# Kernel optimization log

Measured on AMD Instinct MI355X. Metric: run time of the kernel, lower is better.

The kernel has to match this reference:

```python
import jax, jax.numpy as jnp
import numpy as np

N, E, H = 20000, 320000, 5
IND, OUT = 64, 64
D2 = 2 * OUT          # 128
CAT = OUT + D2        # 192
BN_EPS = 1e-5


def _bn(x, g, b, m, v):
    # eval-mode BatchNorm1d
    return (x - m) * jax.lax.rsqrt(v + BN_EPS) * g + b


def _gcn(x, W, b, src, dst, n):
    # PyG GCNConv: add self-loops (already in src/dst), sym-normalized aggregation
    h = x @ W                                             # [N, C]
    deg = jax.ops.segment_sum(jnp.ones_like(dst, dtype=h.dtype), dst, num_segments=n)
    dinv = jnp.where(deg > 0, jax.lax.rsqrt(deg), 0.0)
    norm = dinv[src] * dinv[dst]                          # [E']
    out = jax.ops.segment_sum(h[src] * norm[:, None], dst, num_segments=n)
    return out + b


def _gat(x, W, att_src, att_dst, b, src, dst, n, heads, c):
    # PyG GATConv (concat=False): per-edge attention, segment softmax over dst
    hx = (x @ W).reshape(n, heads, c)                     # [N, H, C]
    a_s = jnp.einsum('nhc,hc->nh', hx, att_src)           # [N, H]
    a_d = jnp.einsum('nhc,hc->nh', hx, att_dst)
    e = jax.nn.leaky_relu(a_s[src] + a_d[dst], 0.2)       # [E', H]
    m = jax.ops.segment_max(e, dst, num_segments=n)       # every node has a self-loop
    w = jnp.exp(e - m[dst])
    den = jax.ops.segment_sum(w, dst, num_segments=n)
    alpha = w / den[dst]                                  # [E', H]
    out = jax.ops.segment_sum(hx[src] * alpha[:, :, None], dst, num_segments=n)  # [N,H,C]
    return out.mean(axis=1) + b


def setup_inputs() -> dict:
    key = jax.random.key(0)
    ks = iter(jax.random.split(key, 64))
    rn = lambda *s: jax.random.normal(next(ks), s, dtype=jnp.float32) * 0.05
    d = {}
    d['x_in'] = jax.random.normal(next(ks), (N, IND), dtype=jnp.float32)
    d['edge_index'] = jax.random.randint(next(ks), (2, E), 0, N, dtype=jnp.int64)
    # nn1: indim -> 2*indim -> outdim -> 2*outdim
    d['nn1_w1'], d['nn1_b1'] = rn(IND, 2 * IND), rn(2 * IND)
    d['nn1_w2'], d['nn1_b2'] = rn(2 * IND, OUT), rn(OUT)
    d['nn1_w3'], d['nn1_b3'] = rn(OUT, D2), rn(D2)
    # batchnorms (eval mode: gamma, beta, running mean/var)
    for name, dim in (('bn0', D2), ('bn1', D2), ('bn2', OUT)):
        d[name + '_g'] = rn(dim) + 1.0
        d[name + '_b'] = rn(dim)
        d[name + '_m'] = rn(dim)
        d[name + '_v'] = jax.random.uniform(next(ks), (dim,), jnp.float32, 0.5, 1.5)
    d['gcn1_w'], d['gcn1_b'] = rn(D2, D2), rn(D2)
    d['gat1_w'] = rn(D2, H * D2)
    d['gat1_as'], d['gat1_ad'], d['gat1_b'] = rn(H, D2), rn(H, D2), rn(D2)
    d['gcn2_w'], d['gcn2_b'] = rn(D2, OUT), rn(OUT)
    d['gat2_w'] = rn(OUT, H * OUT)
    d['gat2_as'], d['gat2_ad'], d['gat2_b'] = rn(H, OUT), rn(H, OUT), rn(OUT)
    # node_pred MLP: 192 -> 96 -> 48 -> 24 -> 1
    d['mlp_w1'], d['mlp_b1'] = rn(CAT, CAT // 2), rn(CAT // 2)
    d['mlp_w2'], d['mlp_b2'] = rn(CAT // 2, CAT // 4), rn(CAT // 4)
    d['mlp_w3'], d['mlp_b3'] = rn(CAT // 4, CAT // 8), rn(CAT // 8)
    d['mlp_w4'], d['mlp_b4'] = rn(CAT // 8, 1), rn(1)
    return d


def reference(x_in, edge_index,
              nn1_w1, nn1_b1, nn1_w2, nn1_b2, nn1_w3, nn1_b3,
              bn0_g, bn0_b, bn0_m, bn0_v,
              gcn1_w, gcn1_b, gat1_w, gat1_as, gat1_ad, gat1_b,
              gcn2_w, gcn2_b, gat2_w, gat2_as, gat2_ad, gat2_b,
              bn1_g, bn1_b, bn1_m, bn1_v,
              bn2_g, bn2_b, bn2_m, bn2_v,
              mlp_w1, mlp_b1, mlp_w2, mlp_b2, mlp_w3, mlp_b3, mlp_w4, mlp_b4):
    n = x_in.shape[0]
    loop = jnp.arange(n, dtype=edge_index.dtype)
    src = jnp.concatenate([edge_index[0], loop])   # self-loops (GCN & GAT defaults)
    dst = jnp.concatenate([edge_index[1], loop])

    sp = jax.nn.softplus
    x = sp(x_in @ nn1_w1 + nn1_b1)
    x = sp(x @ nn1_w2 + nn1_b2)
    x = x @ nn1_w3 + nn1_b3
    x = jax.nn.leaky_relu(_bn(x, bn0_g, bn0_b, bn0_m, bn0_v), 0.01)

    x1 = _gcn(x, gcn1_w, gcn1_b, src, dst, n)
    x1 = _gat(x1, gat1_w, gat1_as, gat1_ad, gat1_b, src, dst, n, H, D2)
    x1 = jax.nn.leaky_relu(_bn(x1, bn1_g, bn1_b, bn1_m, bn1_v), 0.01)
    skip1 = x + x1

    x2 = _gcn(skip1, gcn2_w, gcn2_b, src, dst, n)
    x2 = _gat(x2, gat2_w, gat2_as, gat2_ad, gat2_b, src, dst, n, H, OUT)
    x2 = jax.nn.leaky_relu(_bn(x2, bn2_g, bn2_b, bn2_m, bn2_v), 0.01)

    xf = jnp.concatenate([skip1, x2], axis=1)      # [N, 192]
    h = sp(xf @ mlp_w1 + mlp_b1)
    h = sp(h @ mlp_w2 + mlp_b2)
    h = sp(h @ mlp_w3 + mlp_b3)
    node_probs = jax.nn.sigmoid(h @ mlp_w4 + mlp_b4)   # [N, 1]
    return xf, node_probs
```

## Files before the change

kernel.cpp:

```cpp
#include <hip/hip_runtime.h>
#include <hip/hip_bf16.h>
#include <math.h>
#include <stdint.h>

typedef __hip_bfloat16 bf16;
typedef __hip_bfloat162 bf162;
typedef __attribute__((ext_vector_type(8))) short short8;
typedef __attribute__((ext_vector_type(4))) float f32x4;
#define HEADS 5

static inline long long cdivll(long long a, long long b){ return (a + b - 1) / b; }

__device__ __forceinline__ float b2f(bf16 v){ return __bfloat162float(v); }
__device__ __forceinline__ bf16 f2b(float v){ return __float2bfloat16(v); }
__device__ __forceinline__ short f2bs(float x){ bf16 b = __float2bfloat16(x); return *reinterpret_cast<short*>(&b); }
__device__ __forceinline__ float ldp(const void* p, long long i, int f32){
  return f32 ? ((const float*)p)[i] : b2f(((const bf16*)p)[i]);
}
__device__ __forceinline__ int eidx(const int* ei, long long i, int i64){
  return i64 ? ei[2 * i] : ei[i];
}
__device__ __forceinline__ float lrelu(float x, float a){ return x >= 0.f ? x : a * x; }
__device__ __forceinline__ float splus(float x){ return fmaxf(x, 0.f) + log1pf(expf(-fabsf(x))); }

__global__ void k_detect(const unsigned short* xh, const int* ei, int* flags){
  __shared__ int r0[256], r1[256];
  int t = threadIdx.x;
  int nan_cnt = 0;
  for (int i = t; i < 8192; i += 256){
    unsigned short u = xh[i];
    if (((u >> 7) & 0xFF) == 0xFF) nan_cnt++;
  }
  int odd_nz = 0;
  for (int i = 1 + 2 * t; i < 1024; i += 512) if (ei[i] != 0) odd_nz++;
  r0[t] = nan_cnt; r1[t] = odd_nz; __syncthreads();
  for (int o = 128; o > 0; o >>= 1){
    if (t < o){ r0[t] += r0[t + o]; r1[t] += r1[t + o]; }
    __syncthreads();
  }
  if (t == 0){
    flags[0] = (r0[0] > 0) ? 1 : 0;
    flags[1] = (r1[0] == 0) ? 1 : 0;
  }
}

__global__ void k_stampfill(bf16* out, long long n, float code){
  long long i = (long long)blockIdx.x * blockDim.x + threadIdx.x;
  if (i < n) out[i] = f2b(i == 0 ? code : 0.f);
}

__global__ void k_hist(const int* ei, int E, int N, int* counts, const int* flags){
  int i64 = flags[1];
  int e = blockIdx.x * blockDim.x + threadIdx.x;
  if (e >= E + N) return;
  int d = (e < E) ? eidx(ei, (long long)E + e, i64) : (e - E);
  atomicAdd(&counts[d], 1);
}
__global__ __launch_bounds__(1024) void k_scan(const int* counts, int* rowptr, int N){
  __shared__ int sums[1024];
  int t = threadIdx.x;
  int chunk = (N + 1023) / 1024;
  int start = t * chunk;
  int end = start + chunk; if (end > N) end = N;
  int s = 0;
  for (int i = start; i < end; ++i) s += counts[i];
  sums[t] = s; __syncthreads();
  for (int o = 1; o < 1024; o <<= 1){
    int v = (t >= o) ? sums[t - o] : 0;
    __syncthreads();
    sums[t] += v;
    __syncthreads();
  }
  int run = (t == 0) ? 0 : sums[t - 1];
  for (int i = start; i < end; ++i){ rowptr[i] = run; run += counts[i]; }
  if (t == 0) rowptr[N] = sums[1023];
}
__global__ void k_scatter(const int* ei, int E, int N, const int* rowptr, int* cursor,
                          unsigned short* colu, const int* flags){
  int i64 = flags[1];
  int e = blockIdx.x * blockDim.x + threadIdx.x;
  if (e >= E + N) return;
  int s, d;
  if (e < E){ s = eidx(ei, e, i64); d = eidx(ei, (long long)E + e, i64); }
  else { s = d = e - E; }
  int pos = rowptr[d] + atomicAdd(&cursor[d], 1);
  colu[pos] = (unsigned short)s;
}
__global__ void k_dinv(const int* rowptr, float* dinv, int N){
  int i = blockIdx.x * blockDim.x + threadIdx.x;
  if (i < N) dinv[i] = rsqrtf((float)(rowptr[i + 1] - rowptr[i]));
}

struct PackDesc { const void* W; int K, Kp, C, Cp, off, hk; };
struct PackArgs { PackDesc d[10]; int total; };
__global__ void k_packall(PackArgs P, bf16* WTA, int* cnt, int ncnt, const int* flags){
  int f32 = flags[0];
  int idx = blockIdx.x * blockDim.x + threadIdx.x;
  if (idx >= P.total){
    int z = idx - P.total;
    if (z < ncnt) cnt[z] = 0;
    return;
  }
  int base = 0;
#pragma unroll
  for (int s = 0; s < 10; ++s){
    int sz = P.d[s].Kp * P.d[s].Cp;
    if (idx < base + sz){
      int local = idx - base;
      int c = local / P.d[s].Kp;
      int k = local - c * P.d[s].Kp;
      float v;
      if (P.d[s].hk){
        int h = k / P.d[s].K;
        int kk = k - h * P.d[s].K;
        v = (c < P.d[s].C)
          ? ldp(P.d[s].W, (long long)kk * (P.d[s].hk * P.d[s].C) + h * P.d[s].C + c, f32) : 0.f;
      } else {
        v = (k < P.d[s].K && c < P.d[s].C)
          ? ldp(P.d[s].W, (long long)k * P.d[s].C + c, f32) : 0.f;
      }
      WTA[P.d[s].off + local] = f2b(v);
      return;
    }
    base += sz;
  }
}

__global__ void k_att_fold(const void* w1, const void* as1, const void* ad1,
                           const void* w2, const void* as2, const void* ad2,
                           bf16* wta, const int* flags){
  int f32 = flags[0];
  int idx = blockIdx.x * blockDim.x + threadIdx.x;
  if (idx < 8192){
    int c = idx >> 7, k = idx & 127;
    float v = 0.f;
    if (c < 10){
      int h = (c < 5) ? c : c - 5;
      const void* aw = (c < 5) ? as1 : ad1;
      for (int j = 0; j < 128; ++j)
        v = fmaf(ldp(w1, (long long)k * 640 + h * 128 + j, f32), ldp(aw, h * 128 + j, f32), v);
    }
    wta[186368 + idx] = f2b(v);
  } else if (idx < 12288){
    int l = idx - 8192;
    int c = l >> 6, k = l & 63;
    float v = 0.f;
    if (c < 10){
      int h = (c < 5) ? c : c - 5;
      const void* aw = (c < 5) ? as2 : ad2;
      for (int j = 0; j < 64; ++j)
        v = fmaf(ldp(w2, (long long)k * 320 + h * 64 + j, f32), ldp(aw, h * 64 + j, f32), v);
    }
    wta[194560 + l] = f2b(v);
  }
}

__global__ __launch_bounds__(256) void k_gemm_mfma(
    const void* in, int ik, int ldin, const bf16* WT, int Kp, int ks, const void* bias,
    float* outf, bf16* outb, int N, int C, int ldc, int czero, int mode,
    const void* bg, const void* bb, const void* bm, const void* bv,
    const float* skip, void* out2, int c2off, const int* flags)
{
  __shared__ float red[3][16][64];
  int f32 = flags[0];
  int use_b16 = (ik == 1) || (ik == 2 && !f32);
  int t = threadIdx.x;
  int wave = t >> 6, lane = t & 63;
  int quad = lane >> 4, l15 = lane & 15;
  int nrg = 4 / ks;
  int rowgrp = wave & (nrg - 1);
  int kh = wave / nrg;
  int mbase = blockIdx.x * (16 * nrg) + rowgrp * 16;
  int c0 = blockIdx.y * 64;
  f32x4 acc[4];
#pragma unroll
  for (int j = 0; j < 4; ++j) acc[j] = (f32x4){0.f, 0.f, 0.f, 0.f};

  int m = mbase + l15; if (m > N - 1) m = N - 1;

  int Kseg = Kp / ks;
  int kend = (kh + 1) * Kseg;
  for (int k0 = kh * Kseg; k0 < kend; k0 += 32){
    int ka = k0 + quad * 8;
    short8 af;
    if (use_b16){
      af = *(const short8*)((const bf16*)in + (size_t)m * ldin + ka);
    } else {
      const float* p = (const float*)in + (size_t)m * ldin + ka;
      float4 v0 = *(const float4*)p;
      float4 v1 = *(const float4*)(p + 4);
      af[0] = f2bs(v0.x); af[1] = f2bs(v0.y); af[2] = f2bs(v0.z); af[3] = f2bs(v0.w);
      af[4] = f2bs(v1.x); af[5] = f2bs(v1.y); af[6] = f2bs(v1.z); af[7] = f2bs(v1.w);
    }
#pragma unroll
    for (int j = 0; j < 4; ++j){
      short8 bvv = *(const short8*)(WT + (size_t)(c0 + 16 * j + l15) * Kp + ka);
      acc[j] = __builtin_amdgcn_mfma_f32_16x16x32_bf16(af, bvv, acc[j], 0, 0, 0);
    }
  }

  if (ks > 1){
    if (kh > 0){
      int slot = (kh - 1) * nrg + rowgrp;
#pragma unroll
      for (int j = 0; j < 4; ++j)
#pragma unroll
        for (int r = 0; r < 4; ++r)
          red[slot][quad * 4 + r][16 * j + l15] = acc[j][r];
    }
    __syncthreads();
    if (kh > 0) return;
#pragma unroll
    for (int s = 0; s < 3; ++s){
      if (s < ks - 1){
        int slot = s * nrg + rowgrp;
#pragma unroll
        for (int j = 0; j < 4; ++j)
#pragma unroll
          for (int r = 0; r < 4; ++r)
            acc[j][r] += red[slot][quad * 4 + r][16 * j + l15];
      }
    }
  }

#pragma unroll
  for (int j = 0; j < 4; ++j){
    int c = c0 + 16 * j + l15;
    if (c < C){
      float bi = bias ? ldp(bias, c, f32) : 0.f;
      float g = 0.f, be = 0.f, mm = 0.f, iv = 0.f;
      if (mode == 2){
        g = ldp(bg, c, f32); be = ldp(bb, c, f32); mm = ldp(bm, c, f32);
        iv = rsqrtf(ldp(bv, c, f32) + 1e-5f);
      }
#pragma unroll
      for (int r = 0; r < 4; ++r){
        int n = mbase + quad * 4 + r;
        if (n >= N) continue;
        float y = acc[j][r] + bi;
        if (mode == 1) y = splus(y);
        else if (mode == 2){
          y = (y - mm) * iv * g + be; y = lrelu(y, 0.01f);
          if (skip) y += skip[(size_t)n * ldc + c];
        }
        if (out2){
          size_t o2 = (size_t)n * 192 + c2off + c;
          if (f32) ((float*)out2)[o2] = y; else ((bf16*)out2)[o2] = f2b(y);
        }
        size_t o = (size_t)n * ldc + c;
        if (outb) outb[o] = f2b(y); else if (outf) outf[o] = y;
      }
    } else if (c < czero){
#pragma unroll
      for (int r = 0; r < 4; ++r){
        int n = mbase + quad * 4 + r;
        if (n >= N) continue;
        size_t o = (size_t)n * ldc + c;
        if (outb) outb[o] = f2b(0.f); else if (outf) outf[o] = 0.f;
      }
    }
  }
}

__global__ __launch_bounds__(256) void k_nn1f(
    const void* xin, const bf16* WTA,
    const void* b1, const void* b2, const void* b3,
    const void* g0, const void* bb0, const void* m0, const void* v0,
    float* X, int N, const int* flags)
{
  __shared__ bf16 s1[4][16][136];
  __shared__ bf16 s2[4][16][72];
  int f32 = flags[0];
  int t = threadIdx.x, wave = t >> 6, lane = t & 63;
  int quad = lane >> 4, l15 = lane & 15;
  int mbase = blockIdx.x * 64 + wave * 16;
  int m = mbase + l15; if (m > N - 1) m = N - 1;

  f32x4 a1[8];
#pragma unroll
  for (int j = 0; j < 8; ++j) a1[j] = (f32x4){0.f, 0.f, 0.f, 0.f};
#pragma unroll
  for (int k0 = 0; k0 < 64; k0 += 32){
    int ka = k0 + quad * 8;
    short8 af;
    if (!f32){
      af = *(const short8*)((const bf16*)xin + (size_t)m * 64 + ka);
    } else {
      const float* p = (const float*)xin + (size_t)m * 64 + ka;
      float4 v0 = *(const float4*)p;
      float4 v1 = *(const float4*)(p + 4);
      af[0] = f2bs(v0.x); af[1] = f2bs(v0.y); af[2] = f2bs(v0.z); af[3] = f2bs(v0.w);
      af[4] = f2bs(v1.x); af[5] = f2bs(v1.y); af[6] = f2bs(v1.z); af[7] = f2bs(v1.w);
    }
#pragma unroll
    for (int j = 0; j < 8; ++j){
      short8 bvv = *(const short8*)(WTA + (size_t)(16 * j + l15) * 64 + ka);
      a1[j] = __builtin_amdgcn_mfma_f32_16x16x32_bf16(af, bvv, a1[j], 0, 0, 0);
    }
  }
#pragma unroll
  for (int j = 0; j < 8; ++j){
    int c = 16 * j + l15;
    float bi = ldp(b1, c, f32);
#pragma unroll
    for (int r = 0; r < 4; ++r)
      s1[wave][quad * 4 + r][c] = f2b(splus(a1[j][r] + bi));
  }
  __syncthreads();

  f32x4 a2[4];
#pragma unroll
  for (int j = 0; j < 4; ++j) a2[j] = (f32x4){0.f, 0.f, 0.f, 0.f};
#pragma unroll
  for (int k0 = 0; k0 < 128; k0 += 32){
    int ka = k0 + quad * 8;
    short8 af = *(const short8*)&s1[wave][l15][ka];
#pragma unroll
    for (int j = 0; j < 4; ++j){
      short8 bvv = *(const short8*)(WTA + 8192 + (size_t)(16 * j + l15) * 128 + ka);
      a2[j] = __builtin_amdgcn_mfma_f32_16x16x32_bf16(af, bvv, a2[j], 0, 0, 0);
    }
  }
#pragma unroll
  for (int j = 0; j < 4; ++j){
    int c = 16 * j + l15;
    float bi = ldp(b2, c, f32);
#pragma unroll
    for (int r = 0; r < 4; ++r)
      s2[wave][quad * 4 + r][c] = f2b(splus(a2[j][r] + bi));
  }
  __syncthreads();

  f32x4 a3[8];
#pragma unroll
  for (int j = 0; j < 8; ++j) a3[j] = (f32x4){0.f, 0.f, 0.f, 0.f};
#pragma unroll
  for (int k0 = 0; k0 < 64; k0 += 32){
    int ka = k0 + quad * 8;
    short8 af = *(const short8*)&s2[wave][l15][ka];
#pragma unroll
    for (int j = 0; j < 8; ++j){
      short8 bvv = *(const short8*)(WTA + 16384 + (size_t)(16 * j + l15) * 64 + ka);
      a3[j] = __builtin_amdgcn_mfma_f32_16x16x32_bf16(af, bvv, a3[j], 0, 0, 0);
    }
  }
#pragma unroll
  for (int j = 0; j < 8; ++j){
    int c = 16 * j + l15;
    float bi = ldp(b3, c, f32);
    float g = ldp(g0, c, f32), be = ldp(bb0, c, f32), mm = ldp(m0, c, f32);
    float iv = rsqrtf(ldp(v0, c, f32) + 1e-5f);
#pragma unroll
    for (int r = 0; r < 4; ++r){
      int n = mbase + quad * 4 + r;
      if (n >= N) continue;
      float y = a3[j][r] + bi;
      y = (y - mm) * iv * g + be;
      X[(size_t)n * 128 + c] = lrelu(y, 0.01f);
    }
  }
}

__global__ __launch_bounds__(256) void k_mlpf(
    const void* dout, const bf16* WTA,
    const void* b1, const void* b2, const void* b3,
    const void* w4, const void* b4, void* outfin, int N, const int* flags)
{
  __shared__ bf16 s1[4][16][104];
  __shared__ bf16 s2[4][16][72];
  int f32 = flags[0];
  int t = threadIdx.x, wave = t >> 6, lane = t & 63;
  int quad = lane >> 4, l15 = lane & 15;
  int mbase = blockIdx.x * 64 + wave * 16;
  int m = mbase + l15; if (m > N - 1) m = N - 1;

  f32x4 a1[6];
#pragma unroll
  for (int j = 0; j < 6; ++j) a1[j] = (f32x4){0.f, 0.f, 0.f, 0.f};
#pragma unroll
  for (int k0 = 0; k0 < 192; k0 += 32){
    int ka = k0 + quad * 8;
    short8 af;
    if (!f32){
      af = *(const short8*)((const bf16*)dout + (size_t)m * 192 + ka);
    } else {
      const float* p = (const float*)dout + (size_t)m * 192 + ka;
      float4 v0 = *(const float4*)p;
      float4 v1 = *(const float4*)(p + 4);
      af[0] = f2bs(v0.x); af[1] = f2bs(v0.y); af[2] = f2bs(v0.z); af[3] = f2bs(v0.w);
      af[4] = f2bs(v1.x); af[5] = f2bs(v1.y); af[6] = f2bs(v1.z); af[7] = f2bs(v1.w);
    }
#pragma unroll
    for (int j = 0; j < 6; ++j){
      short8 bvv = *(const short8*)(WTA + 151552 + (size_t)(16 * j + l15) * 192 + ka);
      a1[j] = __builtin_amdgcn_mfma_f32_16x16x32_bf16(af, bvv, a1[j], 0, 0, 0);
    }
  }
#pragma unroll
  for (int j = 0; j < 6; ++j){
    int c = 16 * j + l15;
    float bi = ldp(b1, c, f32);
#pragma unroll
    for (int r = 0; r < 4; ++r)
      s1[wave][quad * 4 + r][c] = f2b(splus(a1[j][r] + bi));
  }
  __syncthreads();

  f32x4 a2[3];
#pragma unroll
  for (int j = 0; j < 3; ++j) a2[j] = (f32x4){0.f, 0.f, 0.f, 0.f};
#pragma unroll
  for (int k0 = 0; k0 < 96; k0 += 32){
    int ka = k0 + quad * 8;
    short8 af = *(const short8*)&s1[wave][l15][ka];
#pragma unroll
    for (int j = 0; j < 3; ++j){
      short8 bvv = *(const short8*)(WTA + 176128 + (size_t)(16 * j + l15) * 96 + ka);
      a2[j] = __builtin_amdgcn_mfma_f32_16x16x32_bf16(af, bvv, a2[j], 0, 0, 0);
    }
  }
#pragma unroll
  for (int j = 0; j < 4; ++j){
    int c = 16 * j + l15;
    if (j < 3){
      float bi = ldp(b2, c, f32);
#pragma unroll
      for (int r = 0; r < 4; ++r)
        s2[wave][quad * 4 + r][c] = f2b(splus(a2[j][r] + bi));
    } else {
#pragma unroll
      for (int r = 0; r < 4; ++r)
        s2[wave][quad * 4 + r][c] = f2b(0.f);
    }
  }
  __syncthreads();

  f32x4 a3[2];
#pragma unroll
  for (int j = 0; j < 2; ++j) a3[j] = (f32x4){0.f, 0.f, 0.f, 0.f};
#pragma unroll
  for (int k0 = 0; k0 < 64; k0 += 32){
    int ka = k0 + quad * 8;
    short8 af = *(const short8*)&s2[wave][l15][ka];
#pragma unroll
    for (int j = 0; j < 2; ++j){
      short8 bvv = *(const short8*)(WTA + 182272 + (size_t)(16 * j + l15) * 64 + ka);
      a3[j] = __builtin_amdgcn_mfma_f32_16x16x32_bf16(af, bvv, a3[j], 0, 0, 0);
    }
  }
  float pr[4] = {0.f, 0.f, 0.f, 0.f};
#pragma unroll
  for (int j = 0; j < 2; ++j){
    int c = 16 * j + l15;
    float w = (c < 24) ? ldp(w4, c, f32) : 0.f;
    float bi = (c < 24) ? ldp(b3, c, f32) : 0.f;
#pragma unroll
    for (int r = 0; r < 4; ++r)
      pr[r] = fmaf(splus(a3[j][r] + bi), w, pr[r]);
  }
#pragma unroll
  for (int r = 0; r < 4; ++r){
#pragma unroll
    for (int o = 1; o < 16; o <<= 1) pr[r] += __shfl_xor(pr[r], o);
    int n = mbase + quad * 4 + r;
    if (l15 == 0 && n < N){
      float p = 1.f / (1.f + expf(-(pr[r] + ldp(b4, 0, f32))));
      long long oi = (long long)N * 192 + n;
      if (f32) ((float*)outfin)[oi] = p; else ((bf16*)outfin)[oi] = f2b(p);
    }
  }
}

__global__ __launch_bounds__(256) void k_gcn_csr(
    const int* rowptr, const unsigned short* colu, const bf16* h,
    const float* dinv, const void* bias, bf16* outb, int N, int C,
    const bf16* watt, float* asd, const int* flags)
{
  int f32 = flags[0];
  int wid = (blockIdx.x * 256 + threadIdx.x) >> 6;
  int lane = threadIdx.x & 63;
  if (wid >= N) return;
  int i0 = rowptr[wid], i1 = rowptr[wid + 1];
  float dr = dinv[wid];
  if (C == 128){
    int coff = lane << 1;
    float ax[4] = {0.f, 0.f, 0.f, 0.f}, ay[4] = {0.f, 0.f, 0.f, 0.f};
    int i = i0;
    for (; i + 3 < i1; i += 4){
      int s[4] = {colu[i], colu[i + 1], colu[i + 2], colu[i + 3]};
#pragma unroll
      for (int e = 0; e < 4; ++e){
        bf162 v = *(const bf162*)(h + (size_t)s[e] * 128 + coff);
        float f = dinv[s[e]];
        ax[e] = fmaf(f, b2f(v.x), ax[e]); ay[e] = fmaf(f, b2f(v.y), ay[e]);
      }
    }
    for (; i < i1; ++i){
      int s0 = colu[i];
      bf162 v = *(const bf162*)(h + (size_t)s0 * 128 + coff);
      float f = dinv[s0];
      ax[0] = fmaf(f, b2f(v.x), ax[0]); ay[0] = fmaf(f, b2f(v.y), ay[0]);
    }
    float sx = (ax[0] + ax[1]) + (ax[2] + ax[3]);
    float sy = (ay[0] + ay[1]) + (ay[2] + ay[3]);
    float vx = sx * dr + ldp(bias, coff, f32);
    float vy = sy * dr + ldp(bias, coff + 1, f32);
    bf162 o; o.x = f2b(vx); o.y = f2b(vy);
    *(bf162*)(outb + (size_t)wid * 128 + coff) = o;
    if (watt){
      float myv = 0.f;
#pragma unroll
      for (int hh = 0; hh < 10; ++hh){
        bf162 w = *(const bf162*)(watt + hh * 128 + coff);
        float p = vx * b2f(w.x) + vy * b2f(w.y);
#pragma unroll
        for (int o2 = 1; o2 < 64; o2 <<= 1) p += __shfl_xor(p, o2);
        if (lane == hh) myv = p;
      }
      if (lane < 10) asd[(size_t)wid * 10 + lane] = myv;
    }
  } else {
    int half = lane >> 5, hl = lane & 31;
    int coff = hl << 1;
    float ax = 0.f, ay = 0.f, bx = 0.f, by = 0.f;
    int i = i0;
    for (; i + 3 < i1; i += 4){
      int sA = colu[i + half], sB = colu[i + 2 + half];
      bf162 vA = *(const bf162*)(h + (size_t)sA * 64 + coff);
      bf162 vB = *(const bf162*)(h + (size_t)sB * 64 + coff);
      float fA = dinv[sA], fB = dinv[sB];
      ax = fmaf(fA, b2f(vA.x), ax); ay = fmaf(fA, b2f(vA.y), ay);
      bx = fmaf(fB, b2f(vB.x), bx); by = fmaf(fB, b2f(vB.y), by);
    }
    for (; i + 1 < i1; i += 2){
      int s = colu[i + half];
      bf162 v = *(const bf162*)(h + (size_t)s * 64 + coff);
      float f = dinv[s];
      ax = fmaf(f, b2f(v.x), ax); ay = fmaf(f, b2f(v.y), ay);
    }
    if (i < i1 && half == 0){
      int s = colu[i];
      bf162 v = *(const bf162*)(h + (size_t)s * 64 + coff);
      float f = dinv[s];
      ax = fmaf(f, b2f(v.x), ax); ay = fmaf(f, b2f(v.y), ay);
    }
    ax += bx; ay += by;
    ax += __shfl_xor(ax, 32);
    ay += __shfl_xor(ay, 32);
    float vx = ax * dr + ldp(bias, coff, f32);
    float vy = ay * dr + ldp(bias, coff + 1, f32);
    if (half == 0){
      bf162 o; o.x = f2b(vx); o.y = f2b(vy);
      *(bf162*)(outb + (size_t)wid * 64 + coff) = o;
    }
    if (watt){
      float myv = 0.f;
#pragma unroll
      for (int hh = 0; hh < 10; ++hh){
        bf162 w = *(const bf162*)(watt + hh * 64 + coff);
        float p = vx * b2f(w.x) + vy * b2f(w.y);
#pragma unroll
        for (int o2 = 1; o2 < 32; o2 <<= 1) p += __shfl_xor(p, o2);
        if (lane == hh) myv = p;
      }
      if (lane < 10) asd[(size_t)wid * 10 + lane] = myv;
    }
  }
}

__global__ __launch_bounds__(256) void k_gat_fused(
    const int* rowptr, const unsigned short* colu, const bf16* bbx,
    const float* asd, bf16* agg, int N, int K)
{
  __shared__ float als[4][HEADS][64];
  __shared__ unsigned short ssrc[4][64];
  int widx = threadIdx.x >> 6;
  int wid = (blockIdx.x * 256 + threadIdx.x) >> 6;
  int lane = threadIdx.x & 63;
  if (wid >= N) return;
  int i0 = rowptr[wid], i1 = rowptr[wid + 1];
  float adr[HEADS];
#pragma unroll
  for (int h = 0; h < HEADS; ++h) adr[h] = asd[(size_t)wid * 10 + 5 + h];
  float m[HEADS];
#pragma unroll
  for (int h = 0; h < HEADS; ++h) m[h] = -1e30f;
  for (int i = i0 + lane; i < i1; i += 64){
    int s = colu[i];
#pragma unroll
    for (int h = 0; h < HEADS; ++h){
      float e = lrelu(asd[(size_t)s * 10 + h] + adr[h], 0.2f);
      m[h] = fmaxf(m[h], e);
    }
  }
#pragma unroll
  for (int h = 0; h < HEADS; ++h)
    for (int o = 32; o > 0; o >>= 1) m[h] = fmaxf(m[h], __shfl_xor(m[h], o));
  float den[HEADS];
#pragma unroll
  for (int h = 0; h < HEADS; ++h) den[h] = 0.f;
  for (int i = i0 + lane; i < i1; i += 64){
    int s = colu[i];
#pragma unroll
    for (int h = 0; h < HEADS; ++h){
      float e = lrelu(asd[(size_t)s * 10 + h] + adr[h], 0.2f);
      den[h] += expf(e - m[h]);
    }
  }
#pragma unroll
  for (int h = 0; h < HEADS; ++h){
    for (int o = 32; o > 0; o >>= 1) den[h] += __shfl_xor(den[h], o);
    den[h] = 1.f / (den[h] * (float)HEADS);
  }
  if (K == 128){
    int coff = lane << 1;
    float ax[HEADS], ay[HEADS];
#pragma unroll
    for (int h = 0; h < HEADS; ++h){ ax[h] = 0.f; ay[h] = 0.f; }
    for (int base = i0; base < i1; base += 64){
      int iend = i1 - base; if (iend > 64) iend = 64;
      int i = base + lane;
      if (i < i1){
        int s = colu[i];
        ssrc[widx][lane] = (unsigned short)s;
#pragma unroll
        for (int h = 0; h < HEADS; ++h){
          float e = lrelu(asd[(size_t)s * 10 + h] + adr[h], 0.2f);
          als[widx][h][lane] = expf(e - m[h]) * den[h];
        }
      }
      asm volatile("s_waitcnt lgkmcnt(0)" ::: "memory");
      int j = 0;
      for (; j + 3 < iend; j += 4){
        int s4[4];
#pragma unroll
        for (int e = 0; e < 4; ++e) s4[e] = ssrc[widx][j + e];
        bf162 v[4];
#pragma unroll
        for (int e = 0; e < 4; ++e) v[e] = *(const bf162*)(bbx + (size_t)s4[e] * 128 + coff);
#pragma unroll
        for (int e = 0; e < 4; ++e){
          float fx = b2f(v[e].x), fy = b2f(v[e].y);
#pragma unroll
          for (int h = 0; h < HEADS; ++h){
            float a = als[widx][h][j + e];
            ax[h] = fmaf(a, fx, ax[h]); ay[h] = fmaf(a, fy, ay[h]);
          }
        }
      }
      for (; j < iend; ++j){
        int s = ssrc[widx][j];
        bf162 v = *(const bf162*)(bbx + (size_t)s * 128 + coff);
        float fx = b2f(v.x), fy = b2f(v.y);
#pragma unroll
        for (int h = 0; h < HEADS; ++h){
          float a = als[widx][h][j];
          ax[h] = fmaf(a, fx, ax[h]); ay[h] = fmaf(a, fy, ay[h]);
        }
      }
    }
#pragma unroll
    for (int h = 0; h < HEADS; ++h){
      bf162 o; o.x = f2b(ax[h]); o.y = f2b(ay[h]);
      *(bf162*)(agg + (size_t)wid * 640 + h * 128 + coff) = o;
    }
  } else {
    int half = lane >> 5, hl = lane & 31;
    int coff = hl << 1;
    float ax[HEADS], ay[HEADS];
#pragma unroll
    for (int h = 0; h < HEADS; ++h){ ax[h] = 0.f; ay[h] = 0.f; }
    for (int base = i0; base < i1; base += 64){
      int iend = i1 - base; if (iend > 64) iend = 64;
      int i = base + lane;
      if (i < i1){
        int s = colu[i];
        ssrc[widx][lane] = (unsigned short)s;
#pragma unroll
        for (int h = 0; h < HEADS; ++h){
          float e = lrelu(asd[(size_t)s * 10 + h] + adr[h], 0.2f);
          als[widx][h][lane] = expf(e - m[h]) * den[h];
        }
      }
      asm volatile("s_waitcnt lgkmcnt(0)" ::: "memory");
      int j = 0;
      for (; j + 3 < iend; j += 4){
        int sA = ssrc[widx][j + half], sB = ssrc[widx][j + 2 + half];
        bf162 vA = *(const bf162*)(bbx + (size_t)sA * 64 + coff);
        bf162 vB = *(const bf162*)(bbx + (size_t)sB * 64 + coff);
        float Ax = b2f(vA.x), Ay = b2f(vA.y), Bx = b2f(vB.x), By = b2f(vB.y);
#pragma unroll
        for (int h = 0; h < HEADS; ++h){
          float aA = als[widx][h][j + half], aB = als[widx][h][j + 2 + half];
          ax[h] = fmaf(aA, Ax, ax[h]); ay[h] = fmaf(aA, Ay, ay[h]);
          ax[h] = fmaf(aB, Bx, ax[h]); ay[h] = fmaf(aB, By, ay[h]);
        }
      }
      for (; j + 1 < iend; j += 2){
        int s = ssrc[widx][j + half];
        bf162 v = *(const bf162*)(bbx + (size_t)s * 64 + coff);
        float fx = b2f(v.x), fy = b2f(v.y);
#pragma unroll
        for (int h = 0; h < HEADS; ++h){
          float a = als[widx][h][j + half];
          ax[h] = fmaf(a, fx, ax[h]); ay[h] = fmaf(a, fy, ay[h]);
        }
      }
      if (j < iend && half == 0){
        int s = ssrc[widx][j];
        bf162 v = *(const bf162*)(bbx + (size_t)s * 64 + coff);
        float fx = b2f(v.x), fy = b2f(v.y);
#pragma unroll
        for (int h = 0; h < HEADS; ++h){
          float a = als[widx][h][j];
          ax[h] = fmaf(a, fx, ax[h]); ay[h] = fmaf(a, fy, ay[h]);
        }
      }
    }
#pragma unroll
    for (int h = 0; h < HEADS; ++h){
      ax[h] += __shfl_xor(ax[h], 32);
      ay[h] += __shfl_xor(ay[h], 32);
    }
    if (half == 0){
#pragma unroll
      for (int h = 0; h < HEADS; ++h){
        bf162 o; o.x = f2b(ax[h]); o.y = f2b(ay[h]);
        *(bf162*)(agg + (size_t)wid * 320 + h * 64 + coff) = o;
      }
    }
  }
}

extern "C" void kernel_launch(void* const* d_in, const int* in_sizes, int n_in,
                              void* d_out, int out_size, void* d_ws, size_t ws_size,
                              hipStream_t stream)
{
  const void* x_in   = d_in[0];
  const int*  ei     = (const int*)d_in[1];
  const void *nn1_w1 = d_in[2], *nn1_b1 = d_in[3], *nn1_w2 = d_in[4], *nn1_b2 = d_in[5];
  const void *nn1_w3 = d_in[6], *nn1_b3 = d_in[7];
  const void *bn0_g = d_in[8],  *bn0_b = d_in[9],  *bn0_m = d_in[10], *bn0_v = d_in[11];
  const void *bn1_g = d_in[12], *bn1_b = d_in[13], *bn1_m = d_in[14], *bn1_v = d_in[15];
  const void *bn2_g = d_in[16], *bn2_b = d_in[17], *bn2_m = d_in[18], *bn2_v = d_in[19];
  const void *gcn1_w = d_in[20], *gcn1_b = d_in[21];
  const void *gat1_w = d_in[22], *gat1_as = d_in[23], *gat1_ad = d_in[24], *gat1_b = d_in[25];
  const void *gcn2_w = d_in[26], *gcn2_b = d_in[27];
  const void *gat2_w = d_in[28], *gat2_as = d_in[29], *gat2_ad = d_in[30], *gat2_b = d_in[31];
  const void *mlp_w1 = d_in[32], *mlp_b1 = d_in[33], *mlp_w2 = d_in[34], *mlp_b2 = d_in[35];
  const void *mlp_w3 = d_in[36], *mlp_b3 = d_in[37], *mlp_w4 = d_in[38], *mlp_b4 = d_in[39];
  (void)n_in;

  const int N  = in_sizes[0] / 64;
  const int E  = in_sizes[1] / 2;
  const int Ep = E + N;
  const int TB = 256;

  if ((long long)out_size != (long long)N * 193 || N > 65535){
    k_stampfill<<<(int)cdivll(out_size, TB), TB, 0, stream>>>((bf16*)d_out, out_size, 8192.f);
    return;
  }
  size_t need = 2900ull * (size_t)N + 500000ull;
  if (ws_size < need){
    k_stampfill<<<(int)cdivll(out_size, TB), TB, 0, stream>>>((bf16*)d_out, out_size, 1024.f);
    return;
  }

  char* wsb = (char*)d_ws;
  int*   FLAGS = (int*)wsb;
  float* X    = (float*)(wsb + 16);
  float* A    = X + (size_t)N * 128;
  float* B    = A + (size_t)N * 128;
  float* DINV = B + (size_t)N * 128;
  float* AS   = DINV + N;
  int*   ROWP = (int*)(AS + (size_t)N * 2 * HEADS);
  unsigned short* COLU = (unsigned short*)(ROWP + N + 1);
  bf16*  HX   = (bf16*)(COLU + ((Ep + 7) & ~7));
  bf16*  WTA  = (bf16*)(((uintptr_t)(HX + (size_t)N * 640) + 15) & ~(uintptr_t)15);
  bf16*  BB   = (bf16*)A;
  int* CNT = (int*)AS;
  int* CUR = CNT + N;
  const int ATT1_OFF = 186368;
  const int ATT2_OFF = 194560;

  k_detect<<<1, 256, 0, stream>>>((const unsigned short*)x_in, ei, FLAGS);

  PackArgs P;
  P.d[0] = {nn1_w1,  64, 64, 128, 128, 0, 0};
  P.d[1] = {nn1_w2, 128,128,  64,  64, 8192, 0};
  P.d[2] = {nn1_w3,  64, 64, 128, 128, 16384, 0};
  P.d[3] = {gcn1_w, 128,128, 128, 128, 24576, 0};
  P.d[4] = {gat1_w, 128,640, 128, 128, 40960, 5};
  P.d[5] = {gcn2_w, 128,128,  64,  64, 122880, 0};
  P.d[6] = {gat2_w,  64,320,  64,  64, 131072, 5};
  P.d[7] = {mlp_w1, 192,192,  96, 128, 151552, 0};
  P.d[8] = {mlp_w2,  96, 96,  48,  64, 176128, 0};
  P.d[9] = {mlp_w3,  48, 64,  24,  64, 182272, 0};
  P.total = 186368;
  k_packall<<<(int)cdivll(P.total + 2 * N, TB), TB, 0, stream>>>(P, WTA, CNT, 2 * N, FLAGS);
  k_att_fold<<<48, 256, 0, stream>>>(gat1_w, gat1_as, gat1_ad, gat2_w, gat2_as, gat2_ad, WTA, FLAGS);

  k_hist<<<(int)cdivll(Ep, TB), TB, 0, stream>>>(ei, E, N, CNT, FLAGS);
  k_scan<<<1, 1024, 0, stream>>>(CNT, ROWP, N);
  k_scatter<<<(int)cdivll(Ep, TB), TB, 0, stream>>>(ei, E, N, ROWP, CUR, COLU, FLAGS);
  k_dinv<<<(int)cdivll(N, TB), TB, 0, stream>>>(ROWP, DINV, N);

  const void* nv = nullptr;
  const float* nf = nullptr;
  auto gemm = [&](const void* in, int ik, int ldin, int off, int Kp, int ks, const void* bias,
                  float* of, bf16* ob, int C, int Cp, int ldc, int czero, int mode,
                  const void* g, const void* b, const void* m, const void* v,
                  const float* skip, void* out2, int c2off){
    dim3 gr((unsigned)cdivll(N, 64 / ks), (unsigned)(Cp / 64));
    k_gemm_mfma<<<gr, 256, 0, stream>>>(in, ik, ldin, WTA + off, Kp, ks, bias, of, ob,
                                        N, C, ldc, czero, mode, g, b, m, v, skip,
                                        out2, c2off, FLAGS);
  };
  int rowsg = (int)cdivll(N, 4);
  int rowsf = (int)cdivll(N, 64);

  k_nn1f<<<rowsf, 256, 0, stream>>>(x_in, WTA, nn1_b1, nn1_b2, nn1_b3,
                                    bn0_g, bn0_b, bn0_m, bn0_v, X, N, FLAGS);

  gemm(X, 0, 128, 24576, 128, 2, nv, nullptr, HX, 128, 128, 128, 0, 0,
       nv, nv, nv, nv, nf, nullptr, 0);
  k_gcn_csr<<<rowsg, 256, 0, stream>>>(ROWP, COLU, HX, DINV, gcn1_b, BB, N, 128,
                                       WTA + ATT1_OFF, AS, FLAGS);

  k_gat_fused<<<rowsg, 256, 0, stream>>>(ROWP, COLU, BB, AS, HX, N, 128);
  gemm(HX, 1, 640, 40960, 640, 4, gat1_b, nullptr, nullptr, 128, 128, 128, 0, 2,
       bn1_g, bn1_b, bn1_m, bn1_v, X, d_out, 0);

  gemm(d_out, 2, 192, 122880, 128, 2, nv, nullptr, HX, 64, 64, 64, 0, 0,
       nv, nv, nv, nv, nf, nullptr, 0);
  k_gcn_csr<<<rowsg, 256, 0, stream>>>(ROWP, COLU, HX, DINV, gcn2_b, BB, N, 64,
                                       WTA + ATT2_OFF, AS, FLAGS);

  k_gat_fused<<<rowsg, 256, 0, stream>>>(ROWP, COLU, BB, AS, HX, N, 64);
  gemm(HX, 1, 320, 131072, 320, 2, gat2_b, nullptr, nullptr, 64, 64, 64, 0, 2,
       bn2_g, bn2_b, bn2_m, bn2_v, nf, d_out, 128);

  k_mlpf<<<rowsf, 256, 0, stream>>>(d_out, WTA, mlp_b1, mlp_b2, mlp_b3,
                                    mlp_w4, mlp_b4, d_out, N, FLAGS);
}
```

Before: 484.1 us.

## Fuse GAT aggregation with head projection, BN and activation in one kernel

The GAT attention aggregation now writes per-node head aggregates into shared memory instead of global memory. The same block then runs the MFMA projection with bias, batch-norm, leaky-relu and skip epilogue, which removes the [N,640]/[N,320] global round trip and one launch per layer. The generic GEMM is replaced by a specialized K=128 projection kernel with fixed two-way K split. In exchange, the fused kernel uses 16 rows per block with a sequential 4-rows-per-wave loop and more shared memory, which may lower occupancy and parallelism in the gather phase.

Result: faster. 468.8 us (-3.2%).

```diff
diff --git a/kernel.cpp b/kernel.cpp
--- a/kernel.cpp
+++ b/kernel.cpp
@@ -155,22 +155,18 @@
   }
 }
 
-__global__ __launch_bounds__(256) void k_gemm_mfma(
-    const void* in, int ik, int ldin, const bf16* WT, int Kp, int ks, const void* bias,
-    float* outf, bf16* outb, int N, int C, int ldc, int czero, int mode,
-    const void* bg, const void* bb, const void* bm, const void* bv,
-    const float* skip, void* out2, int c2off, const int* flags)
+__global__ __launch_bounds__(256) void k_proj128(
+    const void* in, int ik, int ldin, const bf16* WT, bf16* outb,
+    int N, int Cp, const int* flags)
 {
-  __shared__ float red[3][16][64];
+  __shared__ float red[2][16][68];
   int f32 = flags[0];
-  int use_b16 = (ik == 1) || (ik == 2 && !f32);
+  int use_b16 = (ik == 2 && !f32);
   int t = threadIdx.x;
   int wave = t >> 6, lane = t & 63;
   int quad = lane >> 4, l15 = lane & 15;
-  int nrg = 4 / ks;
-  int rowgrp = wave & (nrg - 1);
-  int kh = wave / nrg;
-  int mbase = blockIdx.x * (16 * nrg) + rowgrp * 16;
+  int rowgrp = wave & 1, kh = wave >> 1;
+  int mbase = blockIdx.x * 32 + rowgrp * 16;
   int c0 = blockIdx.y * 64;
   f32x4 acc[4];
 #pragma unroll
@@ -178,10 +174,9 @@
 
   int m = mbase + l15; if (m > N - 1) m = N - 1;
 
-  int Kseg = Kp / ks;
-  int kend = (kh + 1) * Kseg;
-  for (int k0 = kh * Kseg; k0 < kend; k0 += 32){
-    int ka = k0 + quad * 8;
+#pragma unroll
+  for (int ki = 0; ki < 2; ++ki){
+    int ka = kh * 64 + ki * 32 + quad * 8;
     short8 af;
     if (use_b16){
       af = *(const short8*)((const bf16*)in + (size_t)m * ldin + ka);
@@ -194,70 +189,33 @@
     }
 #pragma unroll
     for (int j = 0; j < 4; ++j){
-      short8 bvv = *(const short8*)(WT + (size_t)(c0 + 16 * j + l15) * Kp + ka);
+      short8 bvv = *(const short8*)(WT + (size_t)(c0 + 16 * j + l15) * 128 + ka);
       acc[j] = __builtin_amdgcn_mfma_f32_16x16x32_bf16(af, bvv, acc[j], 0, 0, 0);
     }
   }
 
-  if (ks > 1){
-    if (kh > 0){
-      int slot = (kh - 1) * nrg + rowgrp;
-#pragma unroll
-      for (int j = 0; j < 4; ++j)
-#pragma unroll
-        for (int r = 0; r < 4; ++r)
-          red[slot][quad * 4 + r][16 * j + l15] = acc[j][r];
-    }
-    __syncthreads();
-    if (kh > 0) return;
-#pragma unroll
-    for (int s = 0; s < 3; ++s){
-      if (s < ks - 1){
-        int slot = s * nrg + rowgrp;
-#pragma unroll
-        for (int j = 0; j < 4; ++j)
-#pragma unroll
-          for (int r = 0; r < 4; ++r)
-            acc[j][r] += red[slot][quad * 4 + r][16 * j + l15];
-      }
-    }
-  }
+  if (kh == 1){
+#pragma unroll
+    for (int j = 0; j < 4; ++j)
+#pragma unroll
+      for (int r = 0; r < 4; ++r)
+        red[rowgrp][quad * 4 + r][16 * j + l15] = acc[j][r];
+  }
+  __syncthreads();
+  if (kh == 1) return;
+#pragma unroll
+  for (int j = 0; j < 4; ++j)
+#pragma unroll
+    for (int r = 0; r < 4; ++r)
+      acc[j][r] += red[rowgrp][quad * 4 + r][16 * j + l15];
 
 #pragma unroll
   for (int j = 0; j < 4; ++j){
     int c = c0 + 16 * j + l15;
-    if (c < C){
-      float bi = bias ? ldp(bias, c, f32) : 0.f;
-      float g = 0.f, be = 0.f, mm = 0.f, iv = 0.f;
-      if (mode == 2){
-        g = ldp(bg, c, f32); be = ldp(bb, c, f32); mm = ldp(bm, c, f32);
-        iv = rsqrtf(ldp(bv, c, f32) + 1e-5f);
-      }
-#pragma unroll
-      for (int r = 0; r < 4; ++r){
-        int n = mbase + quad * 4 + r;
-        if (n >= N) continue;
-        float y = acc[j][r] + bi;
-        if (mode == 1) y = splus(y);
-        else if (mode == 2){
-          y = (y - mm) * iv * g + be; y = lrelu(y, 0.01f);
-          if (skip) y += skip[(size_t)n * ldc + c];
-        }
-        if (out2){
-          size_t o2 = (size_t)n * 192 + c2off + c;
-          if (f32) ((float*)out2)[o2] = y; else ((bf16*)out2)[o2] = f2b(y);
-        }
-        size_t o = (size_t)n * ldc + c;
-        if (outb) outb[o] = f2b(y); else if (outf) outf[o] = y;
-      }
-    } else if (c < czero){
-#pragma unroll
-      for (int r = 0; r < 4; ++r){
-        int n = mbase + quad * 4 + r;
-        if (n >= N) continue;
-        size_t o = (size_t)n * ldc + c;
-        if (outb) outb[o] = f2b(0.f); else if (outf) outf[o] = 0.f;
-      }
+#pragma unroll
+    for (int r = 0; r < 4; ++r){
+      int n = mbase + quad * 4 + r;
+      if (n < N) outb[(size_t)n * Cp + c] = f2b(acc[j][r]);
     }
   }
 }
@@ -568,166 +526,214 @@
   }
 }
 
-__global__ __launch_bounds__(256) void k_gat_fused(
+template<int K>
+__global__ __launch_bounds__(256) void k_gat_proj(
     const int* rowptr, const unsigned short* colu, const bf16* bbx,
-    const float* asd, bf16* agg, int N, int K)
+    const float* asd, const bf16* WT, const void* bias,
+    const void* bg, const void* bbp, const void* bm, const void* bv,
+    const float* skip, void* dout, int c2off, int N, const int* flags)
 {
+  constexpr int KP  = HEADS * K;
+  constexpr int AGP = (K == 128) ? 648 : 328;
+  constexpr int C   = K;
+  constexpr int NJ  = C / 64;
+  __shared__ bf16 agg[16][AGP];
   __shared__ float als[4][HEADS][64];
   __shared__ unsigned short ssrc[4][64];
-  int widx = threadIdx.x >> 6;
-  int wid = (blockIdx.x * 256 + threadIdx.x) >> 6;
-  int lane = threadIdx.x & 63;
-  if (wid >= N) return;
-  int i0 = rowptr[wid], i1 = rowptr[wid + 1];
-  float adr[HEADS];
-#pragma unroll
-  for (int h = 0; h < HEADS; ++h) adr[h] = asd[(size_t)wid * 10 + 5 + h];
-  float m[HEADS];
-#pragma unroll
-  for (int h = 0; h < HEADS; ++h) m[h] = -1e30f;
-  for (int i = i0 + lane; i < i1; i += 64){
-    int s = colu[i];
+  int f32 = flags[0];
+  int t = threadIdx.x, wave = t >> 6, lane = t & 63;
+  int quad = lane >> 4, l15 = lane & 15;
+  int rb = blockIdx.x * 16;
+
+  for (int q = 0; q < 4; ++q){
+    int lr = wave * 4 + q;
+    int wid = rb + lr;
+    if (wid >= N) break;
+    int i0 = rowptr[wid], i1 = rowptr[wid + 1];
+    float adr[HEADS];
+#pragma unroll
+    for (int h = 0; h < HEADS; ++h) adr[h] = asd[(size_t)wid * 10 + 5 + h];
+    float mx[HEADS];
+#pragma unroll
+    for (int h = 0; h < HEADS; ++h) mx[h] = -1e30f;
+    for (int i = i0 + lane; i < i1; i += 64){
+      int s = colu[i];
+#pragma unroll
+      for (int h = 0; h < HEADS; ++h){
+        float e = lrelu(asd[(size_t)s * 10 + h] + adr[h], 0.2f);
+        mx[h] = fmaxf(mx[h], e);
+      }
+    }
+#pragma unroll
+    for (int h = 0; h < HEADS; ++h)
+      for (int o = 32; o > 0; o >>= 1) mx[h] = fmaxf(mx[h], __shfl_xor(mx[h], o));
+    float den[HEADS];
+#pragma unroll
+    for (int h = 0; h < HEADS; ++h) den[h] = 0.f;
+    for (int i = i0 + lane; i < i1; i += 64){
+      int s = colu[i];
+#pragma unroll
+      for (int h = 0; h < HEADS; ++h){
+        float e = lrelu(asd[(size_t)s * 10 + h] + adr[h], 0.2f);
+        den[h] += expf(e - mx[h]);
+      }
+    }
 #pragma unroll
     for (int h = 0; h < HEADS; ++h){
-      float e = lrelu(asd[(size_t)s * 10 + h] + adr[h], 0.2f);
-      m[h] = fmaxf(m[h], e);
-    }
-  }
-#pragma unroll
-  for (int h = 0; h < HEADS; ++h)
-    for (int o = 32; o > 0; o >>= 1) m[h] = fmaxf(m[h], __shfl_xor(m[h], o));
-  float den[HEADS];
-#pragma unroll
-  for (int h = 0; h < HEADS; ++h) den[h] = 0.f;
-  for (int i = i0 + lane; i < i1; i += 64){
-    int s = colu[i];
-#pragma unroll
-    for (int h = 0; h < HEADS; ++h){
-      float e = lrelu(asd[(size_t)s * 10 + h] + adr[h], 0.2f);
-      den[h] += expf(e - m[h]);
-    }
-  }
-#pragma unroll
-  for (int h = 0; h < HEADS; ++h){
-    for (int o = 32; o > 0; o >>= 1) den[h] += __shfl_xor(den[h], o);
-    den[h] = 1.f / (den[h] * (float)HEADS);
-  }
-  if (K == 128){
-    int coff = lane << 1;
-    float ax[HEADS], ay[HEADS];
-#pragma unroll
-    for (int h = 0; h < HEADS; ++h){ ax[h] = 0.f; ay[h] = 0.f; }
-    for (int base = i0; base < i1; base += 64){
-      int iend = i1 - base; if (iend > 64) iend = 64;
-      int i = base + lane;
-      if (i < i1){
-        int s = colu[i];
-        ssrc[widx][lane] = (unsigned short)s;
-#pragma unroll
-        for (int h = 0; h < HEADS; ++h){
-          float e = lrelu(asd[(size_t)s * 10 + h] + adr[h], 0.2f);
-          als[widx][h][lane] = expf(e - m[h]) * den[h];
+      for (int o = 32; o > 0; o >>= 1) den[h] += __shfl_xor(den[h], o);
+      den[h] = 1.f / (den[h] * (float)HEADS);
+    }
+    if constexpr (K == 128){
+      int coff = lane << 1;
+      float ax[HEADS], ay[HEADS];
+#pragma unroll
+      for (int h = 0; h < HEADS; ++h){ ax[h] = 0.f; ay[h] = 0.f; }
+      for (int base = i0; base < i1; base += 64){
+        int iend = i1 - base; if (iend > 64) iend = 64;
+        int i = base + lane;
+        if (i < i1){
+          int s = colu[i];
+          ssrc[wave][lane] = (unsigned short)s;
+#pragma unroll
+          for (int h = 0; h < HEADS; ++h){
+            float e = lrelu(asd[(size_t)s * 10 + h] + adr[h], 0.2f);
+            als[wave][h][lane] = expf(e - mx[h]) * den[h];
+          }
         }
-      }
-      asm volatile("s_waitcnt lgkmcnt(0)" ::: "memory");
-      int j = 0;
-      for (; j + 3 < iend; j += 4){
-        int s4[4];
-#pragma unroll
-        for (int e = 0; e < 4; ++e) s4[e] = ssrc[widx][j + e];
-        bf162 v[4];
-#pragma unroll
-        for (int e = 0; e < 4; ++e) v[e] = *(const bf162*)(bbx + (size_t)s4[e] * 128 + coff);
-#pragma unroll
-        for (int e = 0; e < 4; ++e){
-          float fx = b2f(v[e].x), fy = b2f(v[e].y);
+        asm volatile("s_waitcnt lgkmcnt(0)" ::: "memory");
+        int j = 0;
+        for (; j + 3 < iend; j += 4){
+          int s4[4];
+#pragma unroll
+          for (int e = 0; e < 4; ++e) s4[e] = ssrc[wave][j + e];
+          bf162 v[4];
+#pragma unroll
+          for (int e = 0; e < 4; ++e) v[e] = *(const bf162*)(bbx + (size_t)s4[e] * 128 + coff);
+#pragma unroll
+          for (int e = 0; e < 4; ++e){
+            float fx = b2f(v[e].x), fy = b2f(v[e].y);
+#pragma unroll
+            for (int h = 0; h < HEADS; ++h){
+              float a = als[wave][h][j + e];
+              ax[h] = fmaf(a, fx, ax[h]); ay[h] = fmaf(a, fy, ay[h]);
+            }
+          }
+        }
+        for (; j < iend; ++j){
+          int s = ssrc[wave][j];
+          bf162 v = *(const bf162*)(bbx + (size_t)s * 128 + coff);
+          float fx = b2f(v.x), fy = b2f(v.y);
 #pragma unroll
           for (int h = 0; h < HEADS; ++h){
-            float a = als[widx][h][j + e];
+            float a = als[wave][h][j];
             ax[h] = fmaf(a, fx, ax[h]); ay[h] = fmaf(a, fy, ay[h]);
           }
         }
       }
-      for (; j < iend; ++j){
-        int s = ssrc[widx][j];
-        bf162 v = *(const bf162*)(bbx + (size_t)s * 128 + coff);
-        float fx = b2f(v.x), fy = b2f(v.y);
-#pragma unroll
-        for (int h = 0; h < HEADS; ++h){
-          float a = als[widx][h][j];
-          ax[h] = fmaf(a, fx, ax[h]); ay[h] = fmaf(a, fy, ay[h]);
-        }
-      }
-    }
-#pragma unroll
-    for (int h = 0; h < HEADS; ++h){
-      bf162 o; o.x = f2b(ax[h]); o.y = f2b(ay[h]);
-      *(bf162*)(agg + (size_t)wid * 640 + h * 128 + coff) = o;
-    }
-  } else {
-    int half = lane >> 5, hl = lane & 31;
-    int coff = hl << 1;
-    float ax[HEADS], ay[HEADS];
-#pragma unroll
-    for (int h = 0; h < HEADS; ++h){ ax[h] = 0.f; ay[h] = 0.f; }
-    for (int base = i0; base < i1; base += 64){
-      int iend = i1 - base; if (iend > 64) iend = 64;
-      int i = base + lane;
-      if (i < i1){
-        int s = colu[i];
-        ssrc[widx][lane] = (unsigned short)s;
-#pragma unroll
-        for (int h = 0; h < HEADS; ++h){
-          float e = lrelu(asd[(size_t)s * 10 + h] + adr[h], 0.2f);
-          als[widx][h][lane] = expf(e - m[h]) * den[h];
-        }
-      }
-      asm volatile("s_waitcnt lgkmcnt(0)" ::: "memory");
-      int j = 0;
-      for (; j + 3 < iend; j += 4){
-        int sA = ssrc[widx][j + half], sB = ssrc[widx][j + 2 + half];
-        bf162 vA = *(const bf162*)(bbx + (size_t)sA * 64 + coff);
-        bf162 vB = *(const bf162*)(bbx + (size_t)sB * 64 + coff);
-        float Ax = b2f(vA.x), Ay = b2f(vA.y), Bx = b2f(vB.x), By = b2f(vB.y);
-#pragma unroll
-        for (int h = 0; h < HEADS; ++h){
-          float aA = als[widx][h][j + half], aB = als[widx][h][j + 2 + half];
-          ax[h] = fmaf(aA, Ax, ax[h]); ay[h] = fmaf(aA, Ay, ay[h]);
-          ax[h] = fmaf(aB, Bx, ax[h]); ay[h] = fmaf(aB, By, ay[h]);
-        }
-      }
-      for (; j + 1 < iend; j += 2){
-        int s = ssrc[widx][j + half];
-        bf162 v = *(const bf162*)(bbx + (size_t)s * 64 + coff);
-        float fx = b2f(v.x), fy = b2f(v.y);
-#pragma unroll
-        for (int h = 0; h < HEADS; ++h){
-          float a = als[widx][h][j + half];
-          ax[h] = fmaf(a, fx, ax[h]); ay[h] = fmaf(a, fy, ay[h]);
-        }
-      }
-      if (j < iend && half == 0){
-        int s = ssrc[widx][j];
-        bf162 v = *(const bf162*)(bbx + (size_t)s * 64 + coff);
-        float fx = b2f(v.x), fy = b2f(v.y);
-#pragma unroll
-        for (int h = 0; h < HEADS; ++h){
-          float a = als[widx][h][j];
-          ax[h] = fmaf(a, fx, ax[h]); ay[h] = fmaf(a, fy, ay[h]);
-        }
-      }
-    }
-#pragma unroll
-    for (int h = 0; h < HEADS; ++h){
-      ax[h] += __shfl_xor(ax[h], 32);
-      ay[h] += __shfl_xor(ay[h], 32);
-    }
-    if (half == 0){
 #pragma unroll
       for (int h = 0; h < HEADS; ++h){
         bf162 o; o.x = f2b(ax[h]); o.y = f2b(ay[h]);
-        *(bf162*)(agg + (size_t)wid * 320 + h * 64 + coff) = o;
-      }
+        *(bf162*)&agg[lr][h * 128 + coff] = o;
+      }
+    } else {
+      int half = lane >> 5, hl = lane & 31;
+      int coff = hl << 1;
+      float ax[HEADS], ay[HEADS];
+#pragma unroll
+      for (int h = 0; h < HEADS; ++h){ ax[h] = 0.f; ay[h] = 0.f; }
+      for (int base = i0; base < i1; base += 64){
+        int iend = i1 - base; if (iend > 64) iend = 64;
+        int i = base + lane;
+        if (i < i1){
+          int s = colu[i];
+          ssrc[wave][lane] = (unsigned short)s;
+#pragma unroll
+          for (int h = 0; h < HEADS; ++h){
+            float e = lrelu(asd[(size_t)s * 10 + h] + adr[h], 0.2f);
+            als[wave][h][lane] = expf(e - mx[h]) * den[h];
+          }
+        }
+        asm volatile("s_waitcnt lgkmcnt(0)" ::: "memory");
+        int j = 0;
+        for (; j + 3 < iend; j += 4){
+          int sA = ssrc[wave][j + half], sB = ssrc[wave][j + 2 + half];
+          bf162 vA = *(const bf162*)(bbx + (size_t)sA * 64 + coff);
+          bf162 vB = *(const bf162*)(bbx + (size_t)sB * 64 + coff);
+          float Ax = b2f(vA.x), Ay = b2f(vA.y), Bx = b2f(vB.x), By = b2f(vB.y);
+#pragma unroll
+          for (int h = 0; h < HEADS; ++h){
+            float aA = als[wave][h][j + half], aB = als[wave][h][j + 2 + half];
+            ax[h] = fmaf(aA, Ax, ax[h]); ay[h] = fmaf(aA, Ay, ay[h]);
+            ax[h] = fmaf(aB, Bx, ax[h]); ay[h] = fmaf(aB, By, ay[h]);
+          }
+        }
+        for (; j + 1 < iend; j += 2){
+          int s = ssrc[wave][j + half];
+          bf162 v = *(const bf162*)(bbx + (size_t)s * 64 + coff);
+          float fx = b2f(v.x), fy = b2f(v.y);
+#pragma unroll
+          for (int h = 0; h < HEADS; ++h){
+            float a = als[wave][h][j + half];
+            ax[h] = fmaf(a, fx, ax[h]); ay[h] = fmaf(a, fy, ay[h]);
+          }
+        }
+        if (j < iend && half == 0){
+          int s = ssrc[wave][j];
+          bf162 v = *(const bf162*)(bbx + (size_t)s * 64 + coff);
+          float fx = b2f(v.x), fy = b2f(v.y);
+#pragma unroll
+          for (int h = 0; h < HEADS; ++h){
+            float a = als[wave][h][j];
+            ax[h] = fmaf(a, fx, ax[h]); ay[h] = fmaf(a, fy, ay[h]);
+          }
+        }
+      }
+#pragma unroll
+      for (int h = 0; h < HEADS; ++h){
+        ax[h] += __shfl_xor(ax[h], 32);
+        ay[h] += __shfl_xor(ay[h], 32);
+      }
+      if (half == 0){
+#pragma unroll
+        for (int h = 0; h < HEADS; ++h){
+          bf162 o; o.x = f2b(ax[h]); o.y = f2b(ay[h]);
+          *(bf162*)&agg[lr][h * 64 + coff] = o;
+        }
+      }
+    }
+  }
+  __syncthreads();
+
+  f32x4 acc[NJ];
+#pragma unroll
+  for (int j = 0; j < NJ; ++j) acc[j] = (f32x4){0.f, 0.f, 0.f, 0.f};
+  int c0 = wave * (16 * NJ);
+#pragma unroll
+  for (int k0 = 0; k0 < KP; k0 += 32){
+    int ka = k0 + quad * 8;
+    short8 af = *(const short8*)&agg[l15][ka];
+#pragma unroll
+    for (int j = 0; j < NJ; ++j){
+      short8 bvv = *(const short8*)(WT + (size_t)(c0 + 16 * j + l15) * KP + ka);
+      acc[j] = __builtin_amdgcn_mfma_f32_16x16x32_bf16(af, bvv, acc[j], 0, 0, 0);
+    }
+  }
+#pragma unroll
+  for (int j = 0; j < NJ; ++j){
+    int c = c0 + 16 * j + l15;
+    float bi = ldp(bias, c, f32);
+    float g = ldp(bg, c, f32), be = ldp(bbp, c, f32), mm = ldp(bm, c, f32);
+    float iv = rsqrtf(ldp(bv, c, f32) + 1e-5f);
+#pragma unroll
+    for (int r = 0; r < 4; ++r){
+      int n = rb + quad * 4 + r;
+      if (n >= N) continue;
+      float y = acc[j][r] + bi;
+      y = (y - mm) * iv * g + be;
+      y = lrelu(y, 0.01f);
+      if (skip) y += skip[(size_t)n * 128 + c];
+      size_t o = (size_t)n * 192 + c2off + c;
+      if (f32) ((float*)dout)[o] = y; else ((bf16*)dout)[o] = f2b(y);
     }
   }
 }
@@ -805,40 +811,28 @@
   k_scatter<<<(int)cdivll(Ep, TB), TB, 0, stream>>>(ei, E, N, ROWP, CUR, COLU, FLAGS);
   k_dinv<<<(int)cdivll(N, TB), TB, 0, stream>>>(ROWP, DINV, N);
 
-  const void* nv = nullptr;
-  const float* nf = nullptr;
-  auto gemm = [&](const void* in, int ik, int ldin, int off, int Kp, int ks, const void* bias,
-                  float* of, bf16* ob, int C, int Cp, int ldc, int czero, int mode,
-                  const void* g, const void* b, const void* m, const void* v,
-                  const float* skip, void* out2, int c2off){
-    dim3 gr((unsigned)cdivll(N, 64 / ks), (unsigned)(Cp / 64));
-    k_gemm_mfma<<<gr, 256, 0, stream>>>(in, ik, ldin, WTA + off, Kp, ks, bias, of, ob,
-                                        N, C, ldc, czero, mode, g, b, m, v, skip,
-                                        out2, c2off, FLAGS);
-  };
   int rowsg = (int)cdivll(N, 4);
   int rowsf = (int)cdivll(N, 64);
+  int rows16 = (int)cdivll(N, 16);
 
   k_nn1f<<<rowsf, 256, 0, stream>>>(x_in, WTA, nn1_b1, nn1_b2, nn1_b3,
                                     bn0_g, bn0_b, bn0_m, bn0_v, X, N, FLAGS);
 
-  gemm(X, 0, 128, 24576, 128, 2, nv, nullptr, HX, 128, 128, 128, 0, 0,
-       nv, nv, nv, nv, nf, nullptr, 0);
+  k_proj128<<<dim3((unsigned)cdivll(N, 32), 2), 256, 0, stream>>>(
+      X, 0, 128, WTA + 24576, HX, N, 128, FLAGS);
   k_gcn_csr<<<rowsg, 256, 0, stream>>>(ROWP, COLU, HX, DINV, gcn1_b, BB, N, 128,
                                        WTA + ATT1_OFF, AS, FLAGS);
 
-  k_gat_fused<<<rowsg, 256, 0, stream>>>(ROWP, COLU, BB, AS, HX, N, 128);
-  gemm(HX, 1, 640, 40960, 640, 4, gat1_b, nullptr, nullptr, 128, 128, 128, 0, 2,
-       bn1_g, bn1_b, bn1_m, bn1_v, X, d_out, 0);
-
-  gemm(d_out, 2, 192, 122880, 128, 2, nv, nullptr, HX, 64, 64, 64, 0, 0,
-       nv, nv, nv, nv, nf, nullptr, 0);
+  k_gat_proj<128><<<rows16, 256, 0, stream>>>(ROWP, COLU, BB, AS, WTA + 40960, gat1_b,
+      bn1_g, bn1_b, bn1_m, bn1_v, X, d_out, 0, N, FLAGS);
+
+  k_proj128<<<dim3((unsigned)cdivll(N, 32), 1), 256, 0, stream>>>(
+      d_out, 2, 192, WTA + 122880, HX, N, 64, FLAGS);
   k_gcn_csr<<<rowsg, 256, 0, stream>>>(ROWP, COLU, HX, DINV, gcn2_b, BB, N, 64,
                                        WTA + ATT2_OFF, AS, FLAGS);
 
-  k_gat_fused<<<rowsg, 256, 0, stream>>>(ROWP, COLU, BB, AS, HX, N, 64);
-  gemm(HX, 1, 320, 131072, 320, 2, gat2_b, nullptr, nullptr, 64, 64, 64, 0, 2,
-       bn2_g, bn2_b, bn2_m, bn2_v, nf, d_out, 128);
+  k_gat_proj<64><<<rows16, 256, 0, stream>>>(ROWP, COLU, BB, AS, WTA + 131072, gat2_b,
+      bn2_g, bn2_b, bn2_m, bn2_v, nullptr, d_out, 128, N, FLAGS);
 
   k_mlpf<<<rowsf, 256, 0, stream>>>(d_out, WTA, mlp_b1, mlp_b2, mlp_b3,
                                     mlp_w4, mlp_b4, d_out, N, FLAGS);
```
